# Optimization experiments

Measured on AMD Instinct MI355X. Metric: run time of the kernel, lower is better.

## Reference

```python
import jax, jax.numpy as jnp
import numpy as np

B = 128
DIM = 1024


def setup_inputs() -> dict:
    key = jax.random.key(0)
    k1, k2 = jax.random.split(key)
    return {
        "input1": jax.random.normal(k1, (B, DIM), dtype=jnp.float32),
        "input2": jax.random.normal(k2, (B, DIM), dtype=jnp.float32),
    }


def reference(input1, input2):
    # Original torch module computes, via a dim x dim x dim permutation tensor:
    #   cc[b, i] = sum_t input1[b, (i - t) % dim] * input2[b, t]   (circular convolution)
    # then sums over the batch and reshapes to [1, 1, dim].
    dim = input1.shape[1]
    # idx[i, t] = (i - t) mod dim  -> circulant gather of input1
    idx = (jnp.arange(dim)[:, None] - jnp.arange(dim)[None, :]) % dim
    gathered = input1[:, idx]                      # [B, dim, dim]
    cc = jnp.einsum('bit,bt->bi', gathered, input2)  # per-batch circular conv [B, dim]
    sum_rep = jnp.sum(cc, axis=0)                  # [dim]
    return sum_rep[None, None, :]                  # [1, 1, dim]
```

## Files before the change

### kernel.cpp

```cpp
#include <hip/hip_runtime.h>


#define CC_D 1024

__device__ __forceinline__ int swz(int f) {
  return (f & ~7) | ((f + (f >> 3)) & 7);
}

__global__ __launch_bounds__(512, 8) void cc_partial_kernel(
    const float* __restrict__ X, const float* __restrict__ Y,
    float* __restrict__ ws) {
  const int blk    = blockIdx.x;
  const int b      = blk >> 3;
  const int tslice = blk & 7;
  const int tid    = threadIdx.x;
  const int ig     = tid & 127;
  const int ts     = tid >> 7;

  __shared__ __align__(16) float smem[4096];
  float4* sm4 = (float4*)smem;

  if (tid < 256) {
    const float4 v = ((const float4*)(X + b * CC_D))[tid];
    sm4[swz(tid)]       = v;
    sm4[swz(tid + 256)] = v;
  }
  __syncthreads();

  const int ts_u = __builtin_amdgcn_readfirstlane(ts);
  const int t0   = tslice * 128 + ts_u * 32;
  const float* yb = Y + b * CC_D + t0;

  const int f0 = 254 + 2 * ig - (t0 >> 2);

  float W[16];
#pragma unroll
  for (int m = 0; m < 4; ++m) {
    const float4 w = sm4[swz(f0 + m)];
    W[4 * m + 0] = w.x; W[4 * m + 1] = w.y;
    W[4 * m + 2] = w.z; W[4 * m + 3] = w.w;
  }

  float acc[8];
#pragma unroll
  for (int q = 0; q < 8; ++q) acc[q] = 0.f;

#pragma unroll
  for (int g = 0; g < 4; ++g) {
    const float4 ya = ((const float4*)(yb + 8 * g))[0];
    const float4 yc = ((const float4*)(yb + 8 * g))[1];
    const float y[8] = {ya.x, ya.y, ya.z, ya.w, yc.x, yc.y, yc.z, yc.w};

#pragma unroll
    for (int r = 0; r < 8; ++r)
#pragma unroll
      for (int q = 0; q < 8; ++q)
        acc[q] += W[8 + q - r] * y[r];

    if (g < 3) {
#pragma unroll
      for (int j = 0; j < 8; ++j) W[8 + j] = W[j];
      const float4 w0 = sm4[swz(f0 - 2 * (g + 1))];
      const float4 w1 = sm4[swz(f0 - 2 * (g + 1) + 1)];
      W[0] = w0.x; W[1] = w0.y; W[2] = w0.z; W[3] = w0.w;
      W[4] = w1.x; W[5] = w1.y; W[6] = w1.z; W[7] = w1.w;
    }
  }

  __syncthreads();
  float4* st = (float4*)(smem + ts * CC_D + 8 * ig);
  st[0] = make_float4(acc[0], acc[1], acc[2], acc[3]);
  st[1] = make_float4(acc[4], acc[5], acc[6], acc[7]);
  __syncthreads();

  if (tid < 256) {
    float4 s = make_float4(0.f, 0.f, 0.f, 0.f);
#pragma unroll
    for (int sidx = 0; sidx < 4; ++sidx) {
      const float4 v = ((const float4*)smem)[sidx * 256 + tid];
      s.x += v.x; s.y += v.y; s.z += v.z; s.w += v.w;
    }
    ((float4*)ws)[(size_t)tid * 1024 + blk] = s;
  }
}

__global__ __launch_bounds__(256) void cc_reduce_kernel(
    const float* __restrict__ ws, float* __restrict__ out) {
  const int j   = blockIdx.x;
  const int tid = threadIdx.x;
  const int l   = tid & 63;
  const int w   = tid >> 6;

  __shared__ float4 red[4];

  const float4* row = (const float4*)ws + (size_t)j * 1024;
  float4 s = make_float4(0.f, 0.f, 0.f, 0.f);
#pragma unroll
  for (int c = 0; c < 4; ++c) {
    const float4 v = row[(size_t)(c * 256 + tid)];
    s.x += v.x; s.y += v.y; s.z += v.z; s.w += v.w;
  }
#pragma unroll
  for (int o = 32; o > 0; o >>= 1) {
    s.x += __shfl_xor(s.x, o, 64);
    s.y += __shfl_xor(s.y, o, 64);
    s.z += __shfl_xor(s.z, o, 64);
    s.w += __shfl_xor(s.w, o, 64);
  }
  if (l == 0) red[w] = s;
  __syncthreads();

  if (tid == 0) {
    float4 r = red[0];
    r.x += red[1].x + red[2].x + red[3].x;
    r.y += red[1].y + red[2].y + red[3].y;
    r.z += red[1].z + red[2].z + red[3].z;
    r.w += red[1].w + red[2].w + red[3].w;
    ((float4*)out)[j] = r;
  }
}

extern "C" void kernel_launch(void* const* d_in, const int* in_sizes, int n_in,
                              void* d_out, int out_size, void* d_ws,
                              size_t ws_size, hipStream_t stream) {
  const float* X = (const float*)d_in[0];
  const float* Y = (const float*)d_in[1];
  float* out = (float*)d_out;
  float* ws  = (float*)d_ws;

  cc_partial_kernel<<<1024, 512, 0, stream>>>(X, Y, ws);
  cc_reduce_kernel<<<256, 256, 0, stream>>>(ws, out);
}
```

Measured before the change: 65.55 us.

## Repartition circular conv work across batch groups with warp-shuffle t-reduction

Each block now handles 4 batch rows and a 128-output slice with all 1024 t values, where before it handled one batch row and a t-slice. The t-reduction moves from shared memory to wavefront shuffles, and the partial workspace shrinks from 1024 to 32 partials per output. The second kernel becomes a tiny direct sum over 32 batch groups. This cuts workspace traffic and the cost of the reduction kernel, but each block now loads 4 X rows into LDS and runs a 5-step shuffle tree over 8 accumulators, and the grid shrinks to 256 blocks.

```diff
diff --git a/kernel.cpp b/kernel.cpp
--- a/kernel.cpp
+++ b/kernel.cpp
@@ -7,117 +7,98 @@
   return (f & ~7) | ((f + (f >> 3)) & 7);
 }
 
-__global__ __launch_bounds__(512, 8) void cc_partial_kernel(
+__global__ __launch_bounds__(512) void cc_partial_kernel(
     const float* __restrict__ X, const float* __restrict__ Y,
     float* __restrict__ ws) {
-  const int blk    = blockIdx.x;
-  const int b      = blk >> 3;
-  const int tslice = blk & 7;
-  const int tid    = threadIdx.x;
-  const int ig     = tid & 127;
-  const int ts     = tid >> 7;
+  const int blk = blockIdx.x;
+  const int og  = blk >> 5;
+  const int bg  = blk & 31;
+  const int tid = threadIdx.x;
+  const int ig  = tid >> 5;
+  const int ts  = tid & 31;
 
-  __shared__ __align__(16) float smem[4096];
-  float4* sm4 = (float4*)smem;
+  __shared__ __align__(16) float4 sm4[2048];
 
-  if (tid < 256) {
-    const float4 v = ((const float4*)(X + b * CC_D))[tid];
-    sm4[swz(tid)]       = v;
-    sm4[swz(tid + 256)] = v;
+  {
+    const int bb = tid >> 7;
+    const int u0 = tid & 127;
+    const float4* Xr = (const float4*)X + (size_t)(4 * bg + bb) * 256;
+    const float4 v0 = Xr[u0];
+    const float4 v1 = Xr[u0 + 128];
+    float4* R = sm4 + bb * 512;
+    R[swz(u0)]       = v0;
+    R[swz(u0 + 256)] = v0;
+    R[swz(u0 + 128)] = v1;
+    R[swz(u0 + 384)] = v1;
   }
   __syncthreads();
 
-  const int ts_u = __builtin_amdgcn_readfirstlane(ts);
-  const int t0   = tslice * 128 + ts_u * 32;
-  const float* yb = Y + b * CC_D + t0;
-
-  const int f0 = 254 + 2 * ig - (t0 >> 2);
-
-  float W[16];
-#pragma unroll
-  for (int m = 0; m < 4; ++m) {
-    const float4 w = sm4[swz(f0 + m)];
-    W[4 * m + 0] = w.x; W[4 * m + 1] = w.y;
-    W[4 * m + 2] = w.z; W[4 * m + 3] = w.w;
-  }
+  const int f0 = 254 + og * 32 + 2 * ig - 8 * ts;
 
   float acc[8];
 #pragma unroll
   for (int q = 0; q < 8; ++q) acc[q] = 0.f;
 
 #pragma unroll
-  for (int g = 0; g < 4; ++g) {
-    const float4 ya = ((const float4*)(yb + 8 * g))[0];
-    const float4 yc = ((const float4*)(yb + 8 * g))[1];
-    const float y[8] = {ya.x, ya.y, ya.z, ya.w, yc.x, yc.y, yc.z, yc.w};
+  for (int bi = 0; bi < 4; ++bi) {
+    const float4* R = sm4 + bi * 512;
+    const float* yrow = Y + (size_t)(4 * bg + bi) * CC_D + 32 * ts;
+
+    float W[16];
+#pragma unroll
+    for (int m = 0; m < 4; ++m) {
+      const float4 w = R[swz(f0 + m)];
+      W[4 * m + 0] = w.x; W[4 * m + 1] = w.y;
+      W[4 * m + 2] = w.z; W[4 * m + 3] = w.w;
+    }
 
 #pragma unroll
-    for (int r = 0; r < 8; ++r)
+    for (int g = 0; g < 4; ++g) {
+      const float4 ya = ((const float4*)(yrow + 8 * g))[0];
+      const float4 yc = ((const float4*)(yrow + 8 * g))[1];
+      const float y[8] = {ya.x, ya.y, ya.z, ya.w, yc.x, yc.y, yc.z, yc.w};
+
 #pragma unroll
-      for (int q = 0; q < 8; ++q)
-        acc[q] += W[8 + q - r] * y[r];
+      for (int r = 0; r < 8; ++r)
+#pragma unroll
+        for (int q = 0; q < 8; ++q)
+          acc[q] += W[8 + q - r] * y[r];
 
-    if (g < 3) {
+      if (g < 3) {
 #pragma unroll
-      for (int j = 0; j < 8; ++j) W[8 + j] = W[j];
-      const float4 w0 = sm4[swz(f0 - 2 * (g + 1))];
-      const float4 w1 = sm4[swz(f0 - 2 * (g + 1) + 1)];
-      W[0] = w0.x; W[1] = w0.y; W[2] = w0.z; W[3] = w0.w;
-      W[4] = w1.x; W[5] = w1.y; W[6] = w1.z; W[7] = w1.w;
+        for (int j = 0; j < 8; ++j) W[8 + j] = W[j];
+        const float4 w0 = R[swz(f0 - 2 * (g + 1))];
+        const float4 w1 = R[swz(f0 - 2 * (g + 1) + 1)];
+        W[0] = w0.x; W[1] = w0.y; W[2] = w0.z; W[3] = w0.w;
+        W[4] = w1.x; W[5] = w1.y; W[6] = w1.z; W[7] = w1.w;
+      }
     }
   }
 
-  __syncthreads();
-  float4* st = (float4*)(smem + ts * CC_D + 8 * ig);
-  st[0] = make_float4(acc[0], acc[1], acc[2], acc[3]);
-  st[1] = make_float4(acc[4], acc[5], acc[6], acc[7]);
-  __syncthreads();
+#pragma unroll
+  for (int o = 1; o < 32; o <<= 1)
+#pragma unroll
+    for (int q = 0; q < 8; ++q) acc[q] += __shfl_xor(acc[q], o, 64);
 
-  if (tid < 256) {
-    float4 s = make_float4(0.f, 0.f, 0.f, 0.f);
-#pragma unroll
-    for (int sidx = 0; sidx < 4; ++sidx) {
-      const float4 v = ((const float4*)smem)[sidx * 256 + tid];
-      s.x += v.x; s.y += v.y; s.z += v.z; s.w += v.w;
-    }
-    ((float4*)ws)[(size_t)tid * 1024 + blk] = s;
+  if (ts == 0) {
+    const int i4 = og * 32 + 2 * ig;
+    float4* w4 = (float4*)ws;
+    w4[(size_t)bg * 256 + i4]     = make_float4(acc[0], acc[1], acc[2], acc[3]);
+    w4[(size_t)bg * 256 + i4 + 1] = make_float4(acc[4], acc[5], acc[6], acc[7]);
   }
 }
 
-__global__ __launch_bounds__(256) void cc_reduce_kernel(
+__global__ __launch_bounds__(64) void cc_reduce_kernel(
     const float* __restrict__ ws, float* __restrict__ out) {
-  const int j   = blockIdx.x;
-  const int tid = threadIdx.x;
-  const int l   = tid & 63;
-  const int w   = tid >> 6;
-
-  __shared__ float4 red[4];
-
-  const float4* row = (const float4*)ws + (size_t)j * 1024;
+  const int i4 = blockIdx.x * 64 + threadIdx.x;
+  const float4* w4 = (const float4*)ws;
   float4 s = make_float4(0.f, 0.f, 0.f, 0.f);
 #pragma unroll
-  for (int c = 0; c < 4; ++c) {
-    const float4 v = row[(size_t)(c * 256 + tid)];
+  for (int bg = 0; bg < 32; ++bg) {
+    const float4 v = w4[(size_t)bg * 256 + i4];
     s.x += v.x; s.y += v.y; s.z += v.z; s.w += v.w;
   }
-#pragma unroll
-  for (int o = 32; o > 0; o >>= 1) {
-    s.x += __shfl_xor(s.x, o, 64);
-    s.y += __shfl_xor(s.y, o, 64);
-    s.z += __shfl_xor(s.z, o, 64);
-    s.w += __shfl_xor(s.w, o, 64);
-  }
-  if (l == 0) red[w] = s;
-  __syncthreads();
-
-  if (tid == 0) {
-    float4 r = red[0];
-    r.x += red[1].x + red[2].x + red[3].x;
-    r.y += red[1].y + red[2].y + red[3].y;
-    r.z += red[1].z + red[2].z + red[3].z;
-    r.w += red[1].w + red[2].w + red[3].w;
-    ((float4*)out)[j] = r;
-  }
+  ((float4*)out)[i4] = s;
 }
 
 extern "C" void kernel_launch(void* const* d_in, const int* in_sizes, int n_in,
@@ -128,6 +109,6 @@
   float* out = (float*)d_out;
   float* ws  = (float*)d_ws;
 
-  cc_partial_kernel<<<1024, 512, 0, stream>>>(X, Y, ws);
-  cc_reduce_kernel<<<256, 256, 0, stream>>>(ws, out);
+  cc_partial_kernel<<<256, 512, 0, stream>>>(X, Y, ws);
+  cc_reduce_kernel<<<4, 64, 0, stream>>>(ws, out);
 }
```

Result: no change. 65.54 us (-0.0%).
